# Kernel optimization log

Hardware: AMD Instinct MI355X
Metric: run time of the kernel (lower is better)

The kernel has to match this reference:

```python
import jax, jax.numpy as jnp
import numpy as np
import math

HEADS = 16
ROPE_BASE = 10000.0


def _alibi_slopes(n):
    # power-of-2 branch of ALiBiBias._get_slopes (n=16 is a power of 2)
    start = 2.0 ** (-(2.0 ** (-(math.log2(n) - 3))))
    return np.array([start * (start ** i) for i in range(n)], dtype=np.float32)


def _rope_cos_sin(T, head_dim):
    # RotaryPositionalEmbedding: inv_freq over even indices, emb = cat(freqs, freqs)
    inv_freq = 1.0 / (ROPE_BASE ** (jnp.arange(0, head_dim, 2, dtype=jnp.float32) / head_dim))
    t = jnp.arange(T, dtype=jnp.float32)
    f = t[:, None] * inv_freq[None, :]            # (T, head_dim//2)
    emb = jnp.concatenate([f, f], axis=-1)        # (T, head_dim)
    # apply_rotary_pos_emb takes cos/sin of emb then strides [0::2]
    cos = jnp.cos(emb)[:, 0::2]                   # (T, head_dim//2)
    sin = jnp.sin(emb)[:, 0::2]
    return cos, sin


def _apply_rope(x, cos, sin):
    # x: (B,H,T,hd); cos/sin: (T, hd//2)
    x1 = x[..., 0::2]
    x2 = x[..., 1::2]
    r1 = x1 * cos - x2 * sin
    r2 = x2 * cos + x1 * sin
    # interleave back: out[...,0::2]=r1, out[...,1::2]=r2
    return jnp.stack([r1, r2], axis=-1).reshape(x.shape)


def setup_inputs() -> dict:
    key = jax.random.key(0)
    k1, k2, k3, k4 = jax.random.split(key, 4)
    B, T, C = 2, 2048, 1024
    x = jax.random.normal(k1, (B, T, C), dtype=jnp.float32)
    W_qkv = jax.random.normal(k2, (C, 3 * C), dtype=jnp.float32) * 0.02
    W_out = jax.random.normal(k3, (C, C), dtype=jnp.float32) * 0.02
    b_out = jax.random.normal(k4, (C,), dtype=jnp.float32) * 0.02
    return {"x": x, "W_qkv": W_qkv, "W_out": W_out, "b_out": b_out}


def reference(x, W_qkv, W_out, b_out):
    B, T, C = x.shape
    H = HEADS
    hd = C // H

    qkv = (x @ W_qkv).reshape(B, T, 3, H, hd)
    qkv = jnp.transpose(qkv, (2, 0, 3, 1, 4))     # (3, B, H, T, hd)
    q, k, v = qkv[0], qkv[1], qkv[2]

    cos, sin = _rope_cos_sin(T, hd)
    q = _apply_rope(q, cos, sin)
    k = _apply_rope(k, cos, sin)

    scores = jnp.einsum('bhqd,bhkd->bhqk', q, k) / jnp.sqrt(jnp.float32(hd))

    # ALiBi bias: -slope_h * |i - j|
    slopes = jnp.asarray(_alibi_slopes(H))        # (H,)
    pos = jnp.arange(T, dtype=jnp.float32)
    dist = jnp.abs(pos[None, :] - pos[:, None])   # (T, T)
    scores = scores - slopes[None, :, None, None] * dist[None, None, :, :]

    attn = jax.nn.softmax(scores, axis=-1)
    out = jnp.einsum('bhqk,bhkd->bhqd', attn, v)  # (B,H,T,hd)
    out = jnp.transpose(out, (0, 2, 1, 3)).reshape(B, T, C)
    out = out @ W_out + b_out
    return out, attn
```

## Files before the change

kernel.cpp:

```cpp
#include <hip/hip_runtime.h>
#include <hip/hip_bf16.h>

typedef __bf16 bf16_t;
typedef __bf16 bf16x8 __attribute__((ext_vector_type(8)));
typedef __bf16 bf16x4 __attribute__((ext_vector_type(4)));
typedef float floatx4 __attribute__((ext_vector_type(4)));

#define NB 2
#define NT 2048
#define NC 1024
#define NH 16
#define HD 64
#define BT (NB*NT)

#define GLL16(g, l) __builtin_amdgcn_global_load_lds( \
    (const __attribute__((address_space(1))) void*)(g), \
    (__attribute__((address_space(3))) void*)(l), 16, 0, 0)

__global__ void k_cvt_x(const float* __restrict__ x, bf16_t* __restrict__ xb, int n){
  int i = (blockIdx.x*blockDim.x + threadIdx.x)*4;
  if (i >= n) return;
  float4 v = *(const float4*)(x+i);
  bf16_t o[4] = {(bf16_t)v.x,(bf16_t)v.y,(bf16_t)v.z,(bf16_t)v.w};
  *(uint2*)(xb+i) = *(const uint2*)o;
}

__global__ void k_cvt_t(const float* __restrict__ in, bf16_t* __restrict__ out, int K, int N){
  __shared__ float tile[32][33];
  int tid = threadIdx.x;
  int kt = blockIdx.y*32, nt = blockIdx.x*32;
  int row = tid>>3, c4 = (tid&7)*4;
  float4 v = *(const float4*)(in + (size_t)(kt+row)*N + nt + c4);
  tile[row][c4+0]=v.x; tile[row][c4+1]=v.y; tile[row][c4+2]=v.z; tile[row][c4+3]=v.w;
  __syncthreads();
  bf16_t o[4];
  #pragma unroll
  for (int i=0;i<4;i++) o[i] = (bf16_t)tile[c4+i][row];
  *(uint2*)(out + (size_t)(nt+row)*K + kt + c4) = *(const uint2*)o;
}

__global__ void k_trv(const bf16_t* __restrict__ qkv, bf16_t* __restrict__ Vt){
  __shared__ float tile[32][33];
  int tid = threadIdx.x;
  int bh = blockIdx.z; int b = bh>>4, h = bh&15;
  int t0 = blockIdx.y*32, d0 = blockIdx.x*32;
  int row = tid>>3, c4 = (tid&7)*4;
  bf16x4 v = *(const bf16x4*)(qkv + (size_t)(b*NT + t0 + row)*3072 + 2048 + h*HD + d0 + c4);
  #pragma unroll
  for (int i=0;i<4;i++) tile[row][c4+i] = (float)v[i];
  __syncthreads();
  bf16x4 o;
  #pragma unroll
  for (int i=0;i<4;i++) o[i] = (bf16_t)tile[c4+i][row];
  *(bf16x4*)(Vt + ((size_t)bh*HD + d0 + row)*NT + t0 + c4) = o;
}

template<int MI, bool BIAS, bool OUTBF>
__global__ __launch_bounds__(256) void k_gemm(
    const bf16_t* __restrict__ A, const bf16_t* __restrict__ Bt,
    void* __restrict__ Cv, const float* __restrict__ bias, int M, int N, int K){
  constexpr int BM = MI*32;
  __shared__ __align__(16) bf16_t As[BM][64];
  __shared__ __align__(16) bf16_t Bs[128][64];
  int tid = threadIdx.x;
  int wave = tid>>6, lane = tid&63, quad = lane>>4, l15 = lane&15;
  int m0 = blockIdx.y*BM, n0 = blockIdx.x*128;
  int wm = (wave>>1)*(MI*16), wn = (wave&1)*64;
  floatx4 acc[MI][4];
  #pragma unroll
  for(int i=0;i<MI;i++)
    #pragma unroll
    for(int j=0;j<4;j++) acc[i][j] = (floatx4){0.f,0.f,0.f,0.f};
  int srow = lane>>3;
  int sslot = (lane&7) ^ srow;
  const bf16_t* Ag = A  + (size_t)(m0 + wave*(MI*8) + srow)*K + sslot*8;
  const bf16_t* Bg = Bt + (size_t)(n0 + wave*32 + srow)*K + sslot*8;
  int rs = l15 & 7;
  for (int k0=0; k0<K; k0+=64){
    #pragma unroll
    for (int i=0;i<MI;i++)
      GLL16(Ag + (size_t)(i*8)*K + k0, &As[wave*(MI*8) + i*8][0]);
    #pragma unroll
    for (int i=0;i<4;i++)
      GLL16(Bg + (size_t)(i*8)*K + k0, &Bs[wave*32 + i*8][0]);
    __syncthreads();
    bf16x8 af[2][MI], bfr[2][4];
    #pragma unroll
    for (int kk=0;kk<2;kk++){
      #pragma unroll
      for (int mi=0;mi<MI;mi++) af[kk][mi]  = *(const bf16x8*)&As[wm+mi*16+l15][8*((kk*4+quad) ^ rs)];
      #pragma unroll
      for (int ni=0;ni<4;ni++)  bfr[kk][ni] = *(const bf16x8*)&Bs[wn+ni*16+l15][8*((kk*4+quad) ^ rs)];
    }
    #pragma unroll
    for (int kk=0;kk<2;kk++)
      #pragma unroll
      for (int mi=0;mi<MI;mi++)
        #pragma unroll
        for (int ni=0;ni<4;ni++)
          acc[mi][ni] = __builtin_amdgcn_mfma_f32_16x16x32_bf16(af[kk][mi], bfr[kk][ni], acc[mi][ni],0,0,0);
    __syncthreads();
  }
  #pragma unroll
  for (int ni=0;ni<4;ni++){
    int col = n0 + wn + ni*16 + l15;
    float bv = 0.f; if (BIAS) bv = bias[col];
    #pragma unroll
    for (int mi=0;mi<MI;mi++){
      int rowb = m0 + wm + mi*16 + quad*4;
      #pragma unroll
      for (int r=0;r<4;r++){
        float v = acc[mi][ni][r] + bv;
        if (OUTBF) ((bf16_t*)Cv)[(size_t)(rowb+r)*N + col] = (bf16_t)v;
        else       ((float*)Cv)[(size_t)(rowb+r)*N + col]  = v;
      }
    }
  }
}

__global__ void k_rope(const bf16_t* __restrict__ qkv, bf16_t* __restrict__ Qb,
                       bf16_t* __restrict__ Kb){
  int p = blockIdx.x*blockDim.x + threadIdx.x;
  int r = p >> 10;
  int c = (p & 1023)*2;
  int s = c >> 10, rem = c & 1023;
  int h = rem >> 6, d = rem & 63, j = d >> 1;
  int b = r >> 11, t = r & 2047;
  float x1 = (float)qkv[(size_t)r*3072 + c];
  float x2 = (float)qkv[(size_t)r*3072 + c + 1];
  float freq = exp2f(-0.8304820237218406f * (float)(j & 15));
  float ang = (float)t * freq;
  float sn, cs;
  __sincosf(ang, &sn, &cs);
  float o1 = x1*cs - x2*sn;
  float o2 = x2*cs + x1*sn;
  bf16_t* dst = (s==0) ? Qb : Kb;
  bf16_t o[2] = {(bf16_t)o1, (bf16_t)o2};
  *(unsigned int*)(dst + (size_t)((b*NH + h)*NT + t)*HD + d) = *(const unsigned int*)o;
}

__global__ __launch_bounds__(256) void k_attn(
    const bf16_t* __restrict__ Qb, const bf16_t* __restrict__ Kb, const bf16_t* __restrict__ Vtg,
    float* __restrict__ attn, bf16_t* __restrict__ Ob){
  __shared__ __align__(16) bf16_t Ps[4][16][64];
  int tid = threadIdx.x;
  int wave = tid>>6, lane = tid&63, quad = lane>>4, l15 = lane&15;
  int qt = blockIdx.x, bh = blockIdx.y;
  int h = bh & (NH-1);
  const float LOG2E = 1.4426950408889634f;
  float slope2 = exp2f(-0.5f*(float)(h+1)) * LOG2E;
  const float c1 = 0.125f * LOG2E;
  int qbase = qt*64 + wave*16;
  int qpos = qbase + l15;
  const bf16_t* qrow = Qb + ((size_t)bh*NT + qpos)*HD;
  bf16x8 qa0 = *(const bf16x8*)(qrow + quad*8);
  bf16x8 qa1 = *(const bf16x8*)(qrow + 32 + quad*8);
  const bf16_t* kg = Kb  + (size_t)bh*NT*HD;
  const bf16_t* vg = Vtg + (size_t)bh*HD*NT;
  const floatx4 z4 = {0.f,0.f,0.f,0.f};
  int rs = l15 & 7;
  char* psrow = (char*)&Ps[wave][l15][0];

  float lsum = 0.f;
  for (int k0=0;k0<NT;k0+=64){
    #pragma unroll
    for (int nt=0;nt<4;nt++){
      const bf16_t* kr = kg + (size_t)(k0+nt*16+l15)*HD + quad*8;
      bf16x8 ka0 = *(const bf16x8*)(kr);
      bf16x8 ka1 = *(const bf16x8*)(kr + 32);
      floatx4 sv = __builtin_amdgcn_mfma_f32_16x16x32_bf16(ka0, qa0, z4,0,0,0);
      sv = __builtin_amdgcn_mfma_f32_16x16x32_bf16(ka1, qa1, sv,0,0,0);
      float fk = (float)(qpos - (k0 + nt*16 + quad*4));
      #pragma unroll
      for (int r=0;r<4;r++){
        float arg = fmaf(sv[r], c1, -slope2*fabsf(fk - (float)r));
        lsum += exp2f(arg);
      }
    }
  }
  lsum += __shfl_xor(lsum, 16);
  lsum += __shfl_xor(lsum, 32);
  float li = -__log2f(lsum);

  floatx4 oacc[4] = {z4,z4,z4,z4};
  float* attnrow = attn + (size_t)bh*NT*NT + (size_t)qpos*NT;
  for (int k0=0;k0<NT;k0+=64){
    #pragma unroll
    for (int nt=0;nt<4;nt++){
      const bf16_t* kr = kg + (size_t)(k0+nt*16+l15)*HD + quad*8;
      bf16x8 ka0 = *(const bf16x8*)(kr);
      bf16x8 ka1 = *(const bf16x8*)(kr + 32);
      floatx4 sv = __builtin_amdgcn_mfma_f32_16x16x32_bf16(ka0, qa0, z4,0,0,0);
      sv = __builtin_amdgcn_mfma_f32_16x16x32_bf16(ka1, qa1, sv,0,0,0);
      float fk = (float)(qpos - (k0 + nt*16 + quad*4));
      float p[4];
      #pragma unroll
      for (int r=0;r<4;r++){
        float arg = fmaf(sv[r], c1, fmaf(-slope2, fabsf(fk - (float)r), li));
        p[r] = exp2f(arg);
      }
      floatx4 st = {p[0],p[1],p[2],p[3]};
      __builtin_nontemporal_store(st, (floatx4*)(attnrow + k0 + nt*16 + quad*4));
      bf16x4 pb;
      #pragma unroll
      for (int r=0;r<4;r++) pb[r] = (bf16_t)p[r];
      *(bf16x4*)(psrow + (((nt*2 + (quad>>1)) ^ rs)*16 + (quad&1)*8)) = pb;
    }
    #pragma unroll
    for (int ks=0;ks<2;ks++){
      bf16x8 pa = *(const bf16x8*)(psrow + ((ks*4+quad) ^ rs)*16);
      #pragma unroll
      for (int dt=0;dt<4;dt++){
        bf16x8 vb = *(const bf16x8*)(vg + (size_t)(dt*16+l15)*NT + k0 + ks*32 + quad*8);
        oacc[dt] = __builtin_amdgcn_mfma_f32_16x16x32_bf16(pa, vb, oacc[dt],0,0,0);
      }
    }
  }
  int b = bh >> 4;
  #pragma unroll
  for (int dt=0;dt<4;dt++){
    #pragma unroll
    for (int r=0;r<4;r++){
      int t = qbase + quad*4 + r;
      Ob[(size_t)(b*NT + t)*NC + h*HD + dt*16 + l15] = (bf16_t)oacc[dt][r];
    }
  }
}

extern "C" void kernel_launch(void* const* d_in, const int* in_sizes, int n_in,
                              void* d_out, int out_size, void* d_ws, size_t ws_size,
                              hipStream_t stream){
  const float* x    = (const float*)d_in[0];
  const float* Wqkv = (const float*)d_in[1];
  const float* Wout = (const float*)d_in[2];
  const float* bout = (const float*)d_in[3];
  (void)in_sizes; (void)n_in; (void)out_size; (void)ws_size;

  char* ws = (char*)d_ws;
  size_t off = 0;
  auto alloc = [&](size_t elems)->bf16_t* {
    bf16_t* p = (bf16_t*)(ws + off);
    off += ((elems*sizeof(bf16_t) + 255)/256)*256;
    return p;
  };
  bf16_t* Xb   = alloc((size_t)BT*NC);
  bf16_t* Wqt  = alloc((size_t)3*NC*NC);
  bf16_t* Wot  = alloc((size_t)NC*NC);
  bf16_t* QKVb = alloc((size_t)BT*3*NC);
  bf16_t* Qb   = alloc((size_t)NB*NH*NT*HD);
  bf16_t* Kb   = alloc((size_t)NB*NH*NT*HD);
  bf16_t* Vtg  = alloc((size_t)NB*NH*HD*NT);
  bf16_t* Ob   = alloc((size_t)BT*NC);

  k_cvt_x<<<(BT*NC/4)/256, 256, 0, stream>>>(x, Xb, BT*NC);
  k_cvt_t<<<dim3(3*NC/32, NC/32), 256, 0, stream>>>(Wqkv, Wqt, NC, 3*NC);
  k_cvt_t<<<dim3(NC/32,   NC/32), 256, 0, stream>>>(Wout, Wot, NC, NC);
  k_gemm<4,false,true><<<dim3(3*NC/128, BT/128), 256, 0, stream>>>(Xb, Wqt, (void*)QKVb, nullptr, BT, 3*NC, NC);
  k_rope<<<(BT*1024)/256, 256, 0, stream>>>(QKVb, Qb, Kb);
  k_trv<<<dim3(HD/32, NT/32, NB*NH), 256, 0, stream>>>(QKVb, Vtg);
  float* attn = (float*)d_out + (size_t)BT*NC;
  k_attn<<<dim3(NT/64, NB*NH), 256, 0, stream>>>(Qb, Kb, Vtg, attn, Ob);
  k_gemm<2,true,false><<<dim3(NC/128, BT/64), 256, 0, stream>>>(Ob, Wot, d_out, bout, BT, NC, NC);
}
```

Before: 912.0 us.

## Stage K and V tiles in shared memory via global_load_lds with XOR swizzle

Each K and V tile of 64 keys is loaded once per block into LDS with direct global-to-LDS loads, using an XOR swizzle, and then shared by all four waves. Before this, every wave read the same K/V data from global memory separately. The intent is to cut redundant global/L2 traffic by a factor of four. The cost is two block barriers per iteration with no double buffering, so load latency is exposed and the waves must run in lockstep. The kernel is likely dominated by writing the large fp32 attention matrix, which caps the possible gain.

```diff
diff --git a/kernel.cpp b/kernel.cpp
--- a/kernel.cpp
+++ b/kernel.cpp
@@ -142,6 +142,8 @@
 __global__ __launch_bounds__(256) void k_attn(
     const bf16_t* __restrict__ Qb, const bf16_t* __restrict__ Kb, const bf16_t* __restrict__ Vtg,
     float* __restrict__ attn, bf16_t* __restrict__ Ob){
+  __shared__ __align__(16) bf16_t Ks[64][64];
+  __shared__ __align__(16) bf16_t Vs[64][64];
   __shared__ __align__(16) bf16_t Ps[4][16][64];
   int tid = threadIdx.x;
   int wave = tid>>6, lane = tid&63, quad = lane>>4, l15 = lane&15;
@@ -155,8 +157,9 @@
   const bf16_t* qrow = Qb + ((size_t)bh*NT + qpos)*HD;
   bf16x8 qa0 = *(const bf16x8*)(qrow + quad*8);
   bf16x8 qa1 = *(const bf16x8*)(qrow + 32 + quad*8);
-  const bf16_t* kg = Kb  + (size_t)bh*NT*HD;
-  const bf16_t* vg = Vtg + (size_t)bh*HD*NT;
+  int srow = lane>>3, sslot = (lane&7) ^ srow;
+  const bf16_t* kg = Kb  + ((size_t)bh*NT + wave*16 + srow)*HD + sslot*8;
+  const bf16_t* vg = Vtg + ((size_t)bh*HD + wave*16 + srow)*NT + sslot*8;
   const floatx4 z4 = {0.f,0.f,0.f,0.f};
   int rs = l15 & 7;
   char* psrow = (char*)&Ps[wave][l15][0];
@@ -164,12 +167,15 @@
   float lsum = 0.f;
   for (int k0=0;k0<NT;k0+=64){
     #pragma unroll
+    for (int i=0;i<2;i++)
+      GLL16(kg + (size_t)(i*8)*HD + (size_t)k0*HD, &Ks[wave*16 + i*8][0]);
+    __syncthreads();
+    #pragma unroll
     for (int nt=0;nt<4;nt++){
-      const bf16_t* kr = kg + (size_t)(k0+nt*16+l15)*HD + quad*8;
-      bf16x8 ka0 = *(const bf16x8*)(kr);
-      bf16x8 ka1 = *(const bf16x8*)(kr + 32);
-      floatx4 sv = __builtin_amdgcn_mfma_f32_16x16x32_bf16(ka0, qa0, z4,0,0,0);
-      sv = __builtin_amdgcn_mfma_f32_16x16x32_bf16(ka1, qa1, sv,0,0,0);
+      bf16x8 kb0 = *(const bf16x8*)&Ks[nt*16+l15][8*((quad)   ^ rs)];
+      bf16x8 kb1 = *(const bf16x8*)&Ks[nt*16+l15][8*((4+quad) ^ rs)];
+      floatx4 sv = __builtin_amdgcn_mfma_f32_16x16x32_bf16(kb0, qa0, z4,0,0,0);
+      sv = __builtin_amdgcn_mfma_f32_16x16x32_bf16(kb1, qa1, sv,0,0,0);
       float fk = (float)(qpos - (k0 + nt*16 + quad*4));
       #pragma unroll
       for (int r=0;r<4;r++){
@@ -177,6 +183,7 @@
         lsum += exp2f(arg);
       }
     }
+    __syncthreads();
   }
   lsum += __shfl_xor(lsum, 16);
   lsum += __shfl_xor(lsum, 32);
@@ -186,12 +193,17 @@
   float* attnrow = attn + (size_t)bh*NT*NT + (size_t)qpos*NT;
   for (int k0=0;k0<NT;k0+=64){
     #pragma unroll
+    for (int i=0;i<2;i++){
+      GLL16(kg + (size_t)(i*8)*HD + (size_t)k0*HD, &Ks[wave*16 + i*8][0]);
+      GLL16(vg + (size_t)(i*8)*NT + k0,            &Vs[wave*16 + i*8][0]);
+    }
+    __syncthreads();
+    #pragma unroll
     for (int nt=0;nt<4;nt++){
-      const bf16_t* kr = kg + (size_t)(k0+nt*16+l15)*HD + quad*8;
-      bf16x8 ka0 = *(const bf16x8*)(kr);
-      bf16x8 ka1 = *(const bf16x8*)(kr + 32);
-      floatx4 sv = __builtin_amdgcn_mfma_f32_16x16x32_bf16(ka0, qa0, z4,0,0,0);
-      sv = __builtin_amdgcn_mfma_f32_16x16x32_bf16(ka1, qa1, sv,0,0,0);
+      bf16x8 kb0 = *(const bf16x8*)&Ks[nt*16+l15][8*((quad)   ^ rs)];
+      bf16x8 kb1 = *(const bf16x8*)&Ks[nt*16+l15][8*((4+quad) ^ rs)];
+      floatx4 sv = __builtin_amdgcn_mfma_f32_16x16x32_bf16(kb0, qa0, z4,0,0,0);
+      sv = __builtin_amdgcn_mfma_f32_16x16x32_bf16(kb1, qa1, sv,0,0,0);
       float fk = (float)(qpos - (k0 + nt*16 + quad*4));
       float p[4];
       #pragma unroll
@@ -211,10 +223,11 @@
       bf16x8 pa = *(const bf16x8*)(psrow + ((ks*4+quad) ^ rs)*16);
       #pragma unroll
       for (int dt=0;dt<4;dt++){
-        bf16x8 vb = *(const bf16x8*)(vg + (size_t)(dt*16+l15)*NT + k0 + ks*32 + quad*8);
+        bf16x8 vb = *(const bf16x8*)&Vs[dt*16+l15][8*((ks*4+quad) ^ rs)];
         oacc[dt] = __builtin_amdgcn_mfma_f32_16x16x32_bf16(pa, vb, oacc[dt],0,0,0);
       }
     }
+    __syncthreads();
   }
   int b = bh >> 4;
   #pragma unroll
```

New measurement: 747.8 us. 1.22x faster.
